# Performance work log

Measured on AMD Instinct MI355X. Metric: run time of the kernel, lower is better.

## Reference

```python
import jax, jax.numpy as jnp
import numpy as np
from jax import lax

# channels holding diagonal entries of the embedded 4x4 bA (16:32) and bW (32:48)
_DIAG_CH = np.array([16, 21, 26, 31, 32, 37, 42, 47])
_EPS = 1e-4  # Tikhonov term for per-pixel matrix inversion stability


def _interp_matrix(out_n, in_n):
    """Dense 1D bicubic (a=-0.75) align_corners=True interpolation matrix, torch-compatible."""
    if out_n == in_n:
        return jnp.eye(out_n, dtype=jnp.float32)
    a = -0.75
    scale = (in_n - 1) / (out_n - 1)
    src = np.arange(out_n) * scale
    i0 = np.floor(src).astype(np.int64)
    W = np.zeros((out_n, in_n), np.float64)
    rows = np.arange(out_n)
    for k in range(-1, 3):
        t = np.abs(src - (i0 + k))
        w = np.where(t <= 1.0, (a + 2) * t**3 - (a + 3) * t**2 + 1.0,
                     np.where(t < 2.0, a * t**3 - 5 * a * t**2 + 8 * a * t - 4 * a, 0.0))
        np.add.at(W, (rows, np.clip(i0 + k, 0, in_n - 1)), w)  # border replication
    return jnp.asarray(W, jnp.float32)


def _conv(x, w, b):
    y = lax.conv_general_dilated(x, w, (1, 1), 'SAME',
                                 dimension_numbers=('NCHW', 'OIHW', 'NCHW'))
    return y + b[None, :, None, None]


def _leaky(x):
    return jnp.where(x >= 0, x, 0.01 * x)


def _mm_features(x):
    """compute_mm + intensity: x is (b,48,h,w) -> (b,17,h,w)."""
    b, c, h, w = x.shape
    v = jnp.moveaxis(x, 1, -1)                 # (b,h,w,48)
    F = v[..., :16].reshape(b, h, w, 4, 4)     # intensity frames
    A = v[..., 16:32].reshape(b, h, w, 4, 4)   # analyzer calib bA
    Wm = v[..., 32:48].reshape(b, h, w, 4, 4)  # generator calib bW
    eye = _EPS * jnp.eye(4, dtype=x.dtype)
    M = jnp.linalg.inv(A + eye) @ F @ jnp.linalg.inv(Wm + eye)  # M = A^-1 F W^-1
    inten = v[..., :16].mean(-1)[:, None]      # (b,1,h,w)
    m = jnp.moveaxis(M.reshape(b, h, w, 16), -1, 1)  # (b,16,h,w)
    return jnp.concatenate([inten, m], axis=1)


def _maxpool4(x):
    b, c, h, w = x.shape
    return x.reshape(b, c, h // 4, 4, w // 4, 4).max(axis=(3, 5))


def setup_inputs() -> dict:
    key = jax.random.key(0)
    ks = jax.random.split(key, 6)
    x = 0.3 * jax.random.normal(ks[0], (2, 48, 512, 512), jnp.float32)
    diag = jnp.asarray(_DIAG_CH)
    x = x.at[:, diag].add(1.0)  # well-conditioned per-pixel bA/bW ~ I + noise

    def bias48():
        return jnp.zeros((48,), jnp.float32).at[diag].set(1.0)

    iW0 = 0.05 * jax.random.normal(ks[1], (48, 48, 3, 3), jnp.float32)
    iW1 = 0.05 * jax.random.normal(ks[2], (48, 48, 3, 3), jnp.float32)
    oW0 = 0.05 * jax.random.normal(ks[3], (17, 17, 3, 3), jnp.float32)
    oW1 = 0.05 * jax.random.normal(ks[4], (17, 17, 3, 3), jnp.float32)
    return dict(x=x,
                iW0=iW0, iB0=bias48(), iW1=iW1, iB1=bias48(),
                oW0=oW0, oB0=jnp.zeros((17,), jnp.float32),
                oW1=oW1, oB1=jnp.zeros((17,), jnp.float32))


def reference(x, iW0, iB0, iW1, iB1, oW0, oB0, oW1, oB1):
    b, _, h, w = x.shape
    iparams = [(iW0, iB0), (iW1, iB1)]
    oparams = [(oW0, oB0), (oW1, oB1)]
    outs = []
    for lvl in range(2):  # fixed pyramid levels
        x = _leaky(_conv(x, *iparams[lvl]))
        m = _mm_features(x)                       # (b,17,hl,wl)
        Wh = _interp_matrix(h, m.shape[2])
        Ww = _interp_matrix(w, m.shape[3])
        m = jnp.einsum('Oh,bchw->bcOw', Wh, m)    # bicubic upsample rows
        m = jnp.einsum('Pw,bchw->bchP', Ww, m)    # bicubic upsample cols
        m = _leaky(_conv(m, *oparams[lvl]))
        outs.append(m)
        x = _maxpool4(x)
    return jnp.concatenate(outs, axis=1)          # (b,34,h,w)
```

## Files before the change

kernel.cpp:

```cpp
#include <hip/hip_runtime.h>
#include <math.h>


__device__ __forceinline__ float leakyf(float t) { return t >= 0.0f ? t : 0.01f * t; }

template<int CIN, int OCPT, int PX, int TW>
__global__ __launch_bounds__(256, 2)
void conv3x3_leaky(const float* __restrict__ in, const float* __restrict__ wgt,
                   const float* __restrict__ bias, float* __restrict__ out,
                   int H, int W, int COUT, int NG,
                   int in_bstride, int out_bstride, int out_coff)
{
    constexpr int XG     = TW / PX;
    constexpr int TH     = 256 / XG;
    constexpr int COLS   = TW + 2;
    constexpr int ROWS   = TH + 2;
    constexpr int STRIDE = (COLS + 3) & ~3;
    constexpr int TSZ    = ROWS * STRIDE;
    constexpr int ELEMS  = ROWS * COLS;
    constexpr int K      = (ELEMS + 255) / 256;
    constexpr int NV     = PX + 2;

    __shared__ float tile[2 * TSZ];
    __shared__ float wlds[CIN * OCPT * 12];
    __shared__ float blds[OCPT];

    const int tid   = threadIdx.x;
    const int tx    = tid & (XG - 1);
    const int ty    = tid / XG;
    const int g     = blockIdx.z % NG;
    const int b     = blockIdx.z / NG;
    const int obase = g * OCPT;
    const int row0  = blockIdx.y * TH;
    const int col0  = blockIdx.x * TW;
    const int HW    = H * W;

    for (int idx = tid; idx < CIN * OCPT * 9; idx += 256) {
        int c  = idx / (OCPT * 9);
        int r2 = idx - c * (OCPT * 9);
        int o  = r2 / 9;
        int k2 = r2 - o * 9;
        int og = obase + o;
        wlds[(c * OCPT + o) * 12 + k2] = (og < COUT) ? wgt[(og * CIN + c) * 9 + k2] : 0.0f;
    }
    if (tid < OCPT) {
        int og = obase + tid;
        blds[tid] = (og < COUT) ? bias[og] : 0.0f;
    }

    int goff[K], loff[K];
#pragma unroll
    for (int k = 0; k < K; ++k) {
        int idx = tid + k * 256;
        if (idx < ELEMS) {
            int r  = idx / COLS;
            int cc = idx - r * COLS;
            int gr = row0 - 1 + r;
            int gc = col0 - 1 + cc;
            bool v = (gr >= 0 && gr < H && gc >= 0 && gc < W);
            goff[k] = v ? (gr * W + gc) : -1;
            loff[k] = r * STRIDE + cc;
        } else {
            goff[k] = -1;
            loff[k] = -1;
        }
    }

    const float* inb = in + b * in_bstride;

    float sreg[K];
    {
        const float* ic = inb;
#pragma unroll
        for (int k = 0; k < K; ++k) {
            float v = 0.0f;
            if (goff[k] >= 0) v = ic[goff[k]];
            sreg[k] = v;
        }
#pragma unroll
        for (int k = 0; k < K; ++k)
            if (loff[k] >= 0) tile[loff[k]] = sreg[k];
    }
    __syncthreads();

    float acc[OCPT][PX];
#pragma unroll
    for (int o = 0; o < OCPT; ++o)
#pragma unroll
        for (int p = 0; p < PX; ++p) acc[o][p] = 0.0f;

    for (int c = 0; c < CIN; ++c) {
        if (c + 1 < CIN) {
            const float* ic = inb + (c + 1) * HW;
#pragma unroll
            for (int k = 0; k < K; ++k) {
                float v = 0.0f;
                if (goff[k] >= 0) v = ic[goff[k]];
                sreg[k] = v;
            }
        }

        {
            const float* tb = &tile[(c & 1) * TSZ];
            float v[3][NV];
#pragma unroll
            for (int rr = 0; rr < 3; ++rr) {
                const float* tp = tb + (ty + rr) * STRIDE + tx * PX;
                float4 a0 = *(const float4*)tp;
                v[rr][0] = a0.x; v[rr][1] = a0.y; v[rr][2] = a0.z; v[rr][3] = a0.w;
                if constexpr (PX == 8) {
                    float4 a1 = *(const float4*)(tp + 4);
                    float2 a2 = *(const float2*)(tp + 8);
                    v[rr][4] = a1.x; v[rr][5] = a1.y; v[rr][6] = a1.z; v[rr][7] = a1.w;
                    v[rr][8] = a2.x; v[rr][9] = a2.y;
                } else {
                    float2 a1 = *(const float2*)(tp + 4);
                    v[rr][4] = a1.x; v[rr][5] = a1.y;
                }
            }
#pragma unroll
            for (int o = 0; o < OCPT; ++o) {
                const float* wp = &wlds[(c * OCPT + o) * 12];
                float4 w0 = *(const float4*)wp;
                float4 w1 = *(const float4*)(wp + 4);
                float w8 = wp[8];
                float wk[9] = {w0.x, w0.y, w0.z, w0.w, w1.x, w1.y, w1.z, w1.w, w8};
#pragma unroll
                for (int px = 0; px < PX; ++px) {
                    float s = acc[o][px];
#pragma unroll
                    for (int kr = 0; kr < 3; ++kr)
#pragma unroll
                        for (int kc = 0; kc < 3; ++kc)
                            s = fmaf(wk[kr * 3 + kc], v[kr][px + kc], s);
                    acc[o][px] = s;
                }
            }
        }

        if (c + 1 < CIN) {
            float* tb = &tile[((c + 1) & 1) * TSZ];
#pragma unroll
            for (int k = 0; k < K; ++k)
                if (loff[k] >= 0) tb[loff[k]] = sreg[k];
            __syncthreads();
        }
    }

    const int orow = row0 + ty;
    float* outb = out + b * out_bstride;
#pragma unroll
    for (int o = 0; o < OCPT; ++o) {
        int og = obase + o;
        if (og < COUT) {
            float bv = blds[o];
            float r[PX];
#pragma unroll
            for (int p = 0; p < PX; ++p) { float t = acc[o][p] + bv; r[p] = leakyf(t); }
            float* op = outb + ((out_coff + og) * H + orow) * W + col0 + tx * PX;
#pragma unroll
            for (int q = 0; q < PX / 4; ++q)
                *(float4*)(op + 4 * q) = make_float4(r[4*q], r[4*q+1], r[4*q+2], r[4*q+3]);
        }
    }
}

__device__ __forceinline__ void inv4x4(const double* m, double* invOut)
{
    double inv[16];
    inv[0]  =  m[5]*m[10]*m[15] - m[5]*m[11]*m[14] - m[9]*m[6]*m[15] + m[9]*m[7]*m[14] + m[13]*m[6]*m[11] - m[13]*m[7]*m[10];
    inv[4]  = -m[4]*m[10]*m[15] + m[4]*m[11]*m[14] + m[8]*m[6]*m[15] - m[8]*m[7]*m[14] - m[12]*m[6]*m[11] + m[12]*m[7]*m[10];
    inv[8]  =  m[4]*m[9]*m[15]  - m[4]*m[11]*m[13] - m[8]*m[5]*m[15] + m[8]*m[7]*m[13] + m[12]*m[5]*m[11] - m[12]*m[7]*m[9];
    inv[12] = -m[4]*m[9]*m[14]  + m[4]*m[10]*m[13] + m[8]*m[5]*m[14] - m[8]*m[6]*m[13] - m[12]*m[5]*m[10] + m[12]*m[6]*m[9];
    inv[1]  = -m[1]*m[10]*m[15] + m[1]*m[11]*m[14] + m[9]*m[2]*m[15] - m[9]*m[3]*m[14] - m[13]*m[2]*m[11] + m[13]*m[3]*m[10];
    inv[5]  =  m[0]*m[10]*m[15] - m[0]*m[11]*m[14] - m[8]*m[2]*m[15] + m[8]*m[3]*m[14] + m[12]*m[2]*m[11] - m[12]*m[3]*m[10];
    inv[9]  = -m[0]*m[9]*m[15]  + m[0]*m[11]*m[13] + m[8]*m[1]*m[15] - m[8]*m[3]*m[13] - m[12]*m[1]*m[11] + m[12]*m[3]*m[9];
    inv[13] =  m[0]*m[9]*m[14]  - m[0]*m[10]*m[13] - m[8]*m[1]*m[14] + m[8]*m[2]*m[13] + m[12]*m[1]*m[10] - m[12]*m[2]*m[9];
    inv[2]  =  m[1]*m[6]*m[15]  - m[1]*m[7]*m[14]  - m[5]*m[2]*m[15] + m[5]*m[3]*m[14] + m[13]*m[2]*m[7]  - m[13]*m[3]*m[6];
    inv[6]  = -m[0]*m[6]*m[15]  + m[0]*m[7]*m[14]  + m[4]*m[2]*m[15] - m[4]*m[3]*m[14] - m[12]*m[2]*m[7]  + m[12]*m[3]*m[6];
    inv[10] =  m[0]*m[5]*m[15]  - m[0]*m[7]*m[13]  - m[4]*m[1]*m[15] + m[4]*m[3]*m[13] + m[12]*m[1]*m[7]  - m[12]*m[3]*m[5];
    inv[14] = -m[0]*m[5]*m[14]  + m[0]*m[6]*m[13]  + m[4]*m[1]*m[14] - m[4]*m[2]*m[13] - m[12]*m[1]*m[6]  + m[12]*m[2]*m[5];
    inv[3]  = -m[1]*m[6]*m[11]  + m[1]*m[7]*m[10]  + m[5]*m[2]*m[11] - m[5]*m[3]*m[10] - m[9]*m[2]*m[7]   + m[9]*m[3]*m[6];
    inv[7]  =  m[0]*m[6]*m[11]  - m[0]*m[7]*m[10]  - m[4]*m[2]*m[11] + m[4]*m[3]*m[10] + m[8]*m[2]*m[7]   - m[8]*m[3]*m[6];
    inv[11] = -m[0]*m[5]*m[11]  + m[0]*m[7]*m[9]   + m[4]*m[1]*m[11] - m[4]*m[3]*m[9]  - m[8]*m[1]*m[7]   + m[8]*m[3]*m[5];
    inv[15] =  m[0]*m[5]*m[10]  - m[0]*m[6]*m[9]   - m[4]*m[1]*m[10] + m[4]*m[2]*m[9]  + m[8]*m[1]*m[6]   - m[8]*m[2]*m[5];
    double det = m[0]*inv[0] + m[1]*inv[4] + m[2]*inv[8] + m[3]*inv[12];
    det = 1.0 / det;
#pragma unroll
    for (int i = 0; i < 16; ++i) invOut[i] = inv[i] * det;
}

__device__ __forceinline__ void matmul4(const double* A, const double* B, double* C)
{
#pragma unroll
    for (int r = 0; r < 4; ++r)
#pragma unroll
        for (int c = 0; c < 4; ++c) {
            double s = 0.0;
#pragma unroll
            for (int k = 0; k < 4; ++k) s += A[r * 4 + k] * B[k * 4 + c];
            C[r * 4 + c] = s;
        }
}

__global__ __launch_bounds__(256)
void mm_features_kernel(const float* __restrict__ y, float* __restrict__ m, int HW, int n)
{
    int p = blockIdx.x * 256 + threadIdx.x;
    if (p >= n) return;
    int b  = p / HW;
    int sp = p - b * HW;
    const float* base = y + (size_t)b * 48 * HW + sp;

    double A[16];
#pragma unroll
    for (int i = 0; i < 16; ++i) {
        double e = (i == 0 || i == 5 || i == 10 || i == 15) ? 1e-4 : 0.0;
        A[i] = (double)base[(16 + i) * HW] + e;
    }
    double iA[16];
    inv4x4(A, iA);

    double F[16];
    double s = 0.0;
#pragma unroll
    for (int i = 0; i < 16; ++i) { F[i] = (double)base[i * HW]; }
#pragma unroll
    for (int i = 0; i < 16; ++i) s += F[i];
    s *= (1.0 / 16.0);

    double T[16];
    matmul4(iA, F, T);

    double Wm[16];
#pragma unroll
    for (int i = 0; i < 16; ++i) {
        double e = (i == 0 || i == 5 || i == 10 || i == 15) ? 1e-4 : 0.0;
        Wm[i] = (double)base[(32 + i) * HW] + e;
    }
    double iW[16];
    inv4x4(Wm, iW);

    double M[16];
    matmul4(T, iW, M);

    float* ob = m + (size_t)b * 17 * HW + sp;
    ob[0] = (float)s;
#pragma unroll
    for (int i = 0; i < 16; ++i) ob[(1 + i) * HW] = (float)M[i];
}

__global__ __launch_bounds__(256)
void maxpool4_kernel(const float* __restrict__ in, float* __restrict__ out, int n)
{
    int idx = blockIdx.x * 256 + threadIdx.x;
    if (idx >= n) return;
    int ow = idx & 127;
    int oh = (idx >> 7) & 127;
    int ct = idx >> 14;
    const float* p = in + ct * 262144 + (oh * 4) * 512 + ow * 4;
    float mx = -3.4e38f;
#pragma unroll
    for (int r = 0; r < 4; ++r) {
        float4 v = *(const float4*)(p + r * 512);
        mx = fmaxf(mx, fmaxf(fmaxf(v.x, v.y), fmaxf(v.z, v.w)));
    }
    out[idx] = mx;
}

__device__ __forceinline__ double cubw(double t)
{
    const double a = -0.75;
    t = fabs(t);
    if (t <= 1.0) return ((a + 2.0) * t - (a + 3.0)) * t * t + 1.0;
    if (t < 2.0)  return (((t - 5.0) * t + 8.0) * t - 4.0) * a;
    return 0.0;
}

__global__ __launch_bounds__(256)
void bicubic_up4_kernel(const float* __restrict__ src, float* __restrict__ dst, int n)
{
    int idx = blockIdx.x * 256 + threadIdx.x;
    if (idx >= n) return;
    int P  = idx & 511;
    int O  = (idx >> 9) & 511;
    int bc = idx >> 18;
    const double scale = 127.0 / 511.0;
    double sh = O * scale, sw = P * scale;
    int i0 = (int)floor(sh), j0 = (int)floor(sw);
    double wh[4], ww[4];
#pragma unroll
    for (int k = 0; k < 4; ++k) {
        wh[k] = cubw(sh - (double)(i0 + k - 1));
        ww[k] = cubw(sw - (double)(j0 + k - 1));
    }
    const float* sp = src + bc * 16384;
    double acc = 0.0;
#pragma unroll
    for (int ki = 0; ki < 4; ++ki) {
        int ih = min(max(i0 - 1 + ki, 0), 127);
        double rs = 0.0;
#pragma unroll
        for (int kj = 0; kj < 4; ++kj) {
            int iw = min(max(j0 - 1 + kj, 0), 127);
            rs += ww[kj] * (double)sp[ih * 128 + iw];
        }
        acc += wh[ki] * rs;
    }
    dst[idx] = (float)acc;
}

extern "C" void kernel_launch(void* const* d_in, const int* in_sizes, int n_in,
                              void* d_out, int out_size, void* d_ws, size_t ws_size,
                              hipStream_t stream)
{
    const float* x   = (const float*)d_in[0];
    const float* iW0 = (const float*)d_in[1];
    const float* iB0 = (const float*)d_in[2];
    const float* iW1 = (const float*)d_in[3];
    const float* iB1 = (const float*)d_in[4];
    const float* oW0 = (const float*)d_in[5];
    const float* oB0 = (const float*)d_in[6];
    const float* oW1 = (const float*)d_in[7];
    const float* oB1 = (const float*)d_in[8];
    float* out = (float*)d_out;
    float* ws  = (float*)d_ws;

    float* y0 = ws;
    float* m0 = ws + 25165824;
    float* x1 = ws + 34078720;
    float* y1 = ws + 35651584;
    float* m1 = ws + 37224448;
    float* u  = ws;

    conv3x3_leaky<48, 8, 8, 64><<<dim3(8, 16, 12), 256, 0, stream>>>(
        x, iW0, iB0, y0, 512, 512, 48, 6, 48 * 512 * 512, 48 * 512 * 512, 0);
    mm_features_kernel<<<(2 * 512 * 512) / 256, 256, 0, stream>>>(y0, m0, 512 * 512, 2 * 512 * 512);
    conv3x3_leaky<17, 9, 8, 64><<<dim3(8, 16, 4), 256, 0, stream>>>(
        m0, oW0, oB0, out, 512, 512, 17, 2, 17 * 512 * 512, 34 * 512 * 512, 0);
    maxpool4_kernel<<<(2 * 48 * 128 * 128) / 256, 256, 0, stream>>>(y0, x1, 2 * 48 * 128 * 128);

    conv3x3_leaky<48, 4, 4, 32><<<dim3(4, 4, 24), 256, 0, stream>>>(
        x1, iW1, iB1, y1, 128, 128, 48, 12, 48 * 128 * 128, 48 * 128 * 128, 0);
    mm_features_kernel<<<(2 * 128 * 128) / 256, 256, 0, stream>>>(y1, m1, 128 * 128, 2 * 128 * 128);
    bicubic_up4_kernel<<<(2 * 17 * 512 * 512) / 256, 256, 0, stream>>>(m1, u, 2 * 17 * 512 * 512);
    conv3x3_leaky<17, 9, 8, 64><<<dim3(8, 16, 4), 256, 0, stream>>>(
        u, oW1, oB1, out, 512, 512, 17, 2, 17 * 512 * 512, 34 * 512 * 512, 17);
}
```

Before: 692.4 us.

## Read conv weights directly from global memory and reorder grid so groups share input tiles

Drops the per-block LDS staging of weights and bias and reads them straight from global memory inside the channel loop, relying on uniform scalar loads and cache. Moves the output-channel group index into blockIdx.x so blocks covering the same spatial tile with different channel groups run close together, which should improve L2 reuse of the input tile. Raises the launch-bounds occupancy hint from 2 to 3 blocks per SIMD. Risks extra global load latency inside the hot FMA loop and register spills under the tighter register budget.

```diff
diff --git a/kernel.cpp b/kernel.cpp
--- a/kernel.cpp
+++ b/kernel.cpp
@@ -5,7 +5,7 @@
 __device__ __forceinline__ float leakyf(float t) { return t >= 0.0f ? t : 0.01f * t; }
 
 template<int CIN, int OCPT, int PX, int TW>
-__global__ __launch_bounds__(256, 2)
+__global__ __launch_bounds__(256, 3)
 void conv3x3_leaky(const float* __restrict__ in, const float* __restrict__ wgt,
                    const float* __restrict__ bias, float* __restrict__ out,
                    int H, int W, int COUT, int NG,
@@ -22,31 +22,17 @@
     constexpr int NV     = PX + 2;
 
     __shared__ float tile[2 * TSZ];
-    __shared__ float wlds[CIN * OCPT * 12];
-    __shared__ float blds[OCPT];
 
     const int tid   = threadIdx.x;
     const int tx    = tid & (XG - 1);
     const int ty    = tid / XG;
-    const int g     = blockIdx.z % NG;
-    const int b     = blockIdx.z / NG;
+    const int g     = blockIdx.x % NG;
+    const int xt    = blockIdx.x / NG;
+    const int b     = blockIdx.z;
     const int obase = g * OCPT;
     const int row0  = blockIdx.y * TH;
-    const int col0  = blockIdx.x * TW;
+    const int col0  = xt * TW;
     const int HW    = H * W;
-
-    for (int idx = tid; idx < CIN * OCPT * 9; idx += 256) {
-        int c  = idx / (OCPT * 9);
-        int r2 = idx - c * (OCPT * 9);
-        int o  = r2 / 9;
-        int k2 = r2 - o * 9;
-        int og = obase + o;
-        wlds[(c * OCPT + o) * 12 + k2] = (og < COUT) ? wgt[(og * CIN + c) * 9 + k2] : 0.0f;
-    }
-    if (tid < OCPT) {
-        int og = obase + tid;
-        blds[tid] = (og < COUT) ? bias[og] : 0.0f;
-    }
 
     int goff[K], loff[K];
 #pragma unroll
@@ -120,20 +106,22 @@
             }
 #pragma unroll
             for (int o = 0; o < OCPT; ++o) {
-                const float* wp = &wlds[(c * OCPT + o) * 12];
-                float4 w0 = *(const float4*)wp;
-                float4 w1 = *(const float4*)(wp + 4);
-                float w8 = wp[8];
-                float wk[9] = {w0.x, w0.y, w0.z, w0.w, w1.x, w1.y, w1.z, w1.w, w8};
-#pragma unroll
-                for (int px = 0; px < PX; ++px) {
-                    float s = acc[o][px];
-#pragma unroll
-                    for (int kr = 0; kr < 3; ++kr)
-#pragma unroll
-                        for (int kc = 0; kc < 3; ++kc)
-                            s = fmaf(wk[kr * 3 + kc], v[kr][px + kc], s);
-                    acc[o][px] = s;
+                const int og = obase + o;
+                if (og < COUT) {
+                    const float* wp = wgt + ((size_t)og * CIN + c) * 9;
+                    float wk[9];
+#pragma unroll
+                    for (int kk = 0; kk < 9; ++kk) wk[kk] = wp[kk];
+#pragma unroll
+                    for (int px = 0; px < PX; ++px) {
+                        float s = acc[o][px];
+#pragma unroll
+                        for (int kr = 0; kr < 3; ++kr)
+#pragma unroll
+                            for (int kc = 0; kc < 3; ++kc)
+                                s = fmaf(wk[kr * 3 + kc], v[kr][px + kc], s);
+                        acc[o][px] = s;
+                    }
                 }
             }
         }
@@ -153,7 +141,7 @@
     for (int o = 0; o < OCPT; ++o) {
         int og = obase + o;
         if (og < COUT) {
-            float bv = blds[o];
+            float bv = bias[og];
             float r[PX];
 #pragma unroll
             for (int p = 0; p < PX; ++p) { float t = acc[o][p] + bv; r[p] = leakyf(t); }
@@ -333,17 +321,17 @@
     float* m1 = ws + 37224448;
     float* u  = ws;
 
-    conv3x3_leaky<48, 8, 8, 64><<<dim3(8, 16, 12), 256, 0, stream>>>(
+    conv3x3_leaky<48, 8, 8, 64><<<dim3(8 * 6, 16, 2), 256, 0, stream>>>(
         x, iW0, iB0, y0, 512, 512, 48, 6, 48 * 512 * 512, 48 * 512 * 512, 0);
     mm_features_kernel<<<(2 * 512 * 512) / 256, 256, 0, stream>>>(y0, m0, 512 * 512, 2 * 512 * 512);
-    conv3x3_leaky<17, 9, 8, 64><<<dim3(8, 16, 4), 256, 0, stream>>>(
+    conv3x3_leaky<17, 9, 8, 64><<<dim3(8 * 2, 16, 2), 256, 0, stream>>>(
         m0, oW0, oB0, out, 512, 512, 17, 2, 17 * 512 * 512, 34 * 512 * 512, 0);
     maxpool4_kernel<<<(2 * 48 * 128 * 128) / 256, 256, 0, stream>>>(y0, x1, 2 * 48 * 128 * 128);
 
-    conv3x3_leaky<48, 4, 4, 32><<<dim3(4, 4, 24), 256, 0, stream>>>(
+    conv3x3_leaky<48, 4, 4, 32><<<dim3(4 * 12, 4, 2), 256, 0, stream>>>(
         x1, iW1, iB1, y1, 128, 128, 48, 12, 48 * 128 * 128, 48 * 128 * 128, 0);
     mm_features_kernel<<<(2 * 128 * 128) / 256, 256, 0, stream>>>(y1, m1, 128 * 128, 2 * 128 * 128);
     bicubic_up4_kernel<<<(2 * 17 * 512 * 512) / 256, 256, 0, stream>>>(m1, u, 2 * 17 * 512 * 512);
-    conv3x3_leaky<17, 9, 8, 64><<<dim3(8, 16, 4), 256, 0, stream>>>(
+    conv3x3_leaky<17, 9, 8, 64><<<dim3(8 * 2, 16, 2), 256, 0, stream>>>(
         u, oW1, oB1, out, 512, 512, 17, 2, 17 * 512 * 512, 34 * 512 * 512, 17);
 }
```

New measurement: 807.8 us. +16.7%, slower.
